# Performance work log

Measured on AMD Instinct MI355X. Metric: run time of the kernel, lower is better.

## Reference

```python
import jax, jax.numpy as jnp
import numpy as np
from jax import lax

B, T, SDIM, ADIM, HDIM, NH, NBLK, MAXT = 4, 512, 64, 32, 512, 8, 6, 4096
DFF = 4 * HDIM
S = 3 * T  # (num_state_tokens + 1) * context_len
DH = HDIM // NH


def _layernorm(x, g, b, eps=1e-5):
    m = jnp.mean(x, axis=-1, keepdims=True)
    v = jnp.mean((x - m) ** 2, axis=-1, keepdims=True)
    return (x - m) * lax.rsqrt(v + eps) * g + b


def setup_inputs() -> dict:
    key = jax.random.key(0)
    ks = iter(jax.random.split(key, 40))

    def nrm(shape, scale=0.02):
        return jax.random.normal(next(ks), shape, jnp.float32) * scale

    inp = {
        "timesteps": jax.random.randint(next(ks), (B, T), 0, MAXT),
        "state_0": jax.random.normal(next(ks), (B, T, SDIM), jnp.float32),
        "state_1": jax.random.normal(next(ks), (B, T, SDIM), jnp.float32),
        "actions": jax.random.normal(next(ks), (B, T, ADIM), jnp.float32),
        # embeddings / input projections
        "time_emb": nrm((MAXT, HDIM)),
        "Ws": nrm((SDIM, HDIM)), "bs": jnp.zeros((HDIM,), jnp.float32),
        "Wa": nrm((ADIM, HDIM)), "ba": jnp.zeros((HDIM,), jnp.float32),
        # stacked per-block transformer params (leading axis = n_blocks)
        "Wq": nrm((NBLK, HDIM, HDIM)), "bq": jnp.zeros((NBLK, HDIM), jnp.float32),
        "Wk": nrm((NBLK, HDIM, HDIM)), "bk": jnp.zeros((NBLK, HDIM), jnp.float32),
        "Wv": nrm((NBLK, HDIM, HDIM)), "bv": jnp.zeros((NBLK, HDIM), jnp.float32),
        "Wo": nrm((NBLK, HDIM, HDIM)), "bo": jnp.zeros((NBLK, HDIM), jnp.float32),
        "W1": nrm((NBLK, HDIM, DFF)), "b1": jnp.zeros((NBLK, DFF), jnp.float32),
        "W2": nrm((NBLK, DFF, HDIM)), "b2": jnp.zeros((NBLK, HDIM), jnp.float32),
        "ln1_g": jnp.ones((NBLK, HDIM), jnp.float32), "ln1_b": jnp.zeros((NBLK, HDIM), jnp.float32),
        "ln2_g": jnp.ones((NBLK, HDIM), jnp.float32), "ln2_b": jnp.zeros((NBLK, HDIM), jnp.float32),
        # embed layernorm + action head
        "eln_g": jnp.ones((HDIM,), jnp.float32), "eln_b": jnp.zeros((HDIM,), jnp.float32),
        "Wp": nrm((HDIM, ADIM)), "bp": jnp.zeros((ADIM,), jnp.float32),
    }
    return inp


def reference(timesteps, state_0, state_1, actions, time_emb, Ws, bs, Wa, ba,
              Wq, bq, Wk, bk, Wv, bv, Wo, bo, W1, b1, W2, b2,
              ln1_g, ln1_b, ln2_g, ln2_b, eln_g, eln_b, Wp, bp):
    te = time_emb[timesteps]                       # (B, T, H)
    s0 = state_0 @ Ws + bs + te                    # shared state embedding
    s1 = state_1 @ Ws + bs + te
    ae = actions @ Wa + ba + te
    # interleave: (B, T, 3, H) -> (B, 3T, H), token order [s0, s1, a] per timestep
    h = jnp.stack([s0, s1, ae], axis=2).reshape(B, S, HDIM)
    h = _layernorm(h, eln_g, eln_b)

    causal = jnp.tril(jnp.ones((S, S), dtype=bool))
    scale = 1.0 / float(DH) ** 0.5

    def block(x, p):
        wq, bq_, wk, bk_, wv, bv_, wo, bo_, w1, b1_, w2, b2_, g1, be1, g2, be2 = p
        q = (x @ wq + bq_).reshape(B, S, NH, DH)
        k = (x @ wk + bk_).reshape(B, S, NH, DH)
        v = (x @ wv + bv_).reshape(B, S, NH, DH)
        scores = jnp.einsum('bihd,bjhd->bhij', q, k) * scale
        scores = jnp.where(causal, scores, -jnp.inf)
        attn = jax.nn.softmax(scores, axis=-1)
        ctx = jnp.einsum('bhij,bjhd->bihd', attn, v).reshape(B, S, HDIM)
        x = x + (ctx @ wo + bo_)
        x = _layernorm(x, g1, be1)
        mlp = jax.nn.gelu(x @ w1 + b1_, approximate=False) @ w2 + b2_
        x = _layernorm(x + mlp, g2, be2)
        return x, None

    h, _ = lax.scan(block, h,
                    (Wq, bq, Wk, bk, Wv, bv, Wo, bo, W1, b1, W2, b2,
                     ln1_g, ln1_b, ln2_g, ln2_b))

    h = h.reshape(B, T, 3, HDIM)                   # (B, T, num_tokens, H)
    act_in = h[:, :, 1]                            # token index -2 = last state token
    return act_in @ Wp + bp                        # (B, T, act_dim)
```

## Files before the change

### kernel.cpp

```cpp
#include <hip/hip_runtime.h>
#include <hip/hip_bf16.h>
#include <math.h>

#define BB 4
#define TT 512
#define SDIM 64
#define ADIM 32
#define HDIM 512
#define NH 8
#define NBLK 6
#define DFF 2048
#define SS 1536
#define DH 64
#define MS (BB*SS)

typedef __attribute__((ext_vector_type(8))) __bf16 bf16x8;
typedef __attribute__((ext_vector_type(4))) float f32x4;

__device__ __forceinline__ __bf16 f2b(float x) { return (__bf16)x; }

__device__ __forceinline__ void gll16(const void* g, void* l) {
    __builtin_amdgcn_global_load_lds(
        (const __attribute__((address_space(1))) unsigned int*)g,
        (__attribute__((address_space(3))) unsigned int*)l, 16, 0, 0);
}

__global__ __launch_bounds__(512) void embed_ln_kernel(
    const int* __restrict__ timesteps,
    const float* __restrict__ state0, const float* __restrict__ state1,
    const float* __restrict__ actions, const float* __restrict__ time_emb,
    const float* __restrict__ Ws, const float* __restrict__ bs,
    const float* __restrict__ Wa, const float* __restrict__ ba,
    const float* __restrict__ eg, const float* __restrict__ eb,
    __bf16* __restrict__ h_bf)
{
    __shared__ float xs[8][64];
    __shared__ float acc_s[8][512];
    __shared__ int tss[8];
    int c = blockIdx.x, t = blockIdx.y, b = blockIdx.z;
    int i0 = c * 8;
    int tid = threadIdx.x;
    int K = (t == 2) ? ADIM : SDIM;
    int ksh = (t == 2) ? 5 : 6;
    const float* W    = (t == 2) ? Wa : Ws;
    const float* bias = (t == 2) ? ba : bs;
    const float* src  = (t == 0) ? state0  + ((size_t)(b*TT + i0)) * SDIM
                      : (t == 1) ? state1  + ((size_t)(b*TT + i0)) * SDIM
                                 : actions + ((size_t)(b*TT + i0)) * ADIM;

    if (tid < 8) tss[tid] = timesteps[b*TT + i0 + tid];
    for (int idx = tid; idx < 8 * K; idx += 512) {
        int r = idx >> ksh, kk = idx & (K - 1);
        xs[r][kk] = src[r * K + kk];
    }
    __syncthreads();

    float acc[8];
    #pragma unroll
    for (int r = 0; r < 8; ++r)
        acc[r] = bias[tid] + time_emb[(size_t)tss[r] * HDIM + tid];
    for (int kk = 0; kk < K; ++kk) {
        float w = W[(size_t)kk * HDIM + tid];
        #pragma unroll
        for (int r = 0; r < 8; ++r) acc[r] += xs[r][kk] * w;
    }
    #pragma unroll
    for (int r = 0; r < 8; ++r) acc_s[r][tid] = acc[r];
    __syncthreads();

    int w = tid >> 6, lane = tid & 63;
    float4 p0 = *(const float4*)&acc_s[w][lane * 8];
    float4 p1 = *(const float4*)&acc_s[w][lane * 8 + 4];
    float v[8] = {p0.x, p0.y, p0.z, p0.w, p1.x, p1.y, p1.z, p1.w};
    float s = 0.f, sq = 0.f;
    #pragma unroll
    for (int u = 0; u < 8; ++u) { s += v[u]; sq += v[u] * v[u]; }
    #pragma unroll
    for (int off = 1; off < 64; off <<= 1) { s += __shfl_xor(s, off); sq += __shfl_xor(sq, off); }
    float mean = s * (1.f / HDIM);
    float var  = sq * (1.f / HDIM) - mean * mean;
    float inv  = rsqrtf(var + 1e-5f);
    float4 g0 = *(const float4*)(eg + lane * 8), g1 = *(const float4*)(eg + lane * 8 + 4);
    float4 b0 = *(const float4*)(eb + lane * 8), b1 = *(const float4*)(eb + lane * 8 + 4);
    float gg[8] = {g0.x, g0.y, g0.z, g0.w, g1.x, g1.y, g1.z, g1.w};
    float bbv[8] = {b0.x, b0.y, b0.z, b0.w, b1.x, b1.y, b1.z, b1.w};
    __bf16 o8[8];
    #pragma unroll
    for (int u = 0; u < 8; ++u) o8[u] = f2b((v[u] - mean) * inv * gg[u] + bbv[u]);
    int row = b * SS + (i0 + w) * 3 + t;
    *(uint4*)(h_bf + (size_t)row * HDIM + lane * 8) = *(uint4*)o8;
}

__global__ __launch_bounds__(256) void ln_add2_kernel(
    __bf16* __restrict__ h_bf, const __bf16* __restrict__ ya,
    const __bf16* __restrict__ yb,
    const float* __restrict__ g, const float* __restrict__ bvec)
{
    int w = threadIdx.x >> 6, lane = threadIdx.x & 63;
    int row = blockIdx.x * 4 + w;
    size_t base = (size_t)row * HDIM + lane * 8;
    bf16x8 h8 = *(const bf16x8*)(h_bf + base);
    bf16x8 a8 = *(const bf16x8*)(ya + base);
    bf16x8 b8 = *(const bf16x8*)(yb + base);
    float v[8], s = 0.f, sq = 0.f;
    #pragma unroll
    for (int u = 0; u < 8; ++u) {
        v[u] = (float)h8[u] + (float)a8[u] + (float)b8[u];
        s += v[u]; sq += v[u] * v[u];
    }
    #pragma unroll
    for (int off = 1; off < 64; off <<= 1) { s += __shfl_xor(s, off); sq += __shfl_xor(sq, off); }
    float mean = s * (1.f / HDIM);
    float var  = sq * (1.f / HDIM) - mean * mean;
    float inv  = rsqrtf(var + 1e-5f);
    float4 g0 = *(const float4*)(g + lane * 8), g1 = *(const float4*)(g + lane * 8 + 4);
    float4 b0 = *(const float4*)(bvec + lane * 8), b1 = *(const float4*)(bvec + lane * 8 + 4);
    float gg[8] = {g0.x, g0.y, g0.z, g0.w, g1.x, g1.y, g1.z, g1.w};
    float bbv[8] = {b0.x, b0.y, b0.z, b0.w, b1.x, b1.y, b1.z, b1.w};
    __bf16 o8[8];
    #pragma unroll
    for (int u = 0; u < 8; ++u) o8[u] = f2b((v[u] - mean) * inv * gg[u] + bbv[u]);
    *(uint4*)(h_bf + base) = *(uint4*)o8;
}

__global__ __launch_bounds__(256) void pack_kernel(
    const float* __restrict__ Wq, const float* __restrict__ Wk,
    const float* __restrict__ Wv, const float* __restrict__ Wo,
    const float* __restrict__ W1, const float* __restrict__ W2,
    const float* __restrict__ bq_, const float* __restrict__ bk_, const float* __restrict__ bv_,
    __bf16* __restrict__ wqkvT, __bf16* __restrict__ woT,
    __bf16* __restrict__ w1T, __bf16* __restrict__ w2T, float* __restrict__ biasq)
{
    int lyr = blockIdx.y;
    const float* wq = Wq + (size_t)lyr * HDIM * HDIM;
    const float* wk = Wk + (size_t)lyr * HDIM * HDIM;
    const float* wv = Wv + (size_t)lyr * HDIM * HDIM;
    const float* wo = Wo + (size_t)lyr * HDIM * HDIM;
    const float* w1 = W1 + (size_t)lyr * HDIM * DFF;
    const float* w2 = W2 + (size_t)lyr * DFF * HDIM;
    const float* bqL = bq_ + (size_t)lyr * HDIM;
    const float* bkL = bk_ + (size_t)lyr * HDIM;
    const float* bvL = bv_ + (size_t)lyr * HDIM;
    wqkvT += (size_t)lyr * 1536 * 512;
    woT   += (size_t)lyr * 512 * 512;
    w1T   += (size_t)lyr * 2048 * 512;
    w2T   += (size_t)lyr * 512 * 2048;
    biasq += (size_t)lyr * 1536;

    int bid = blockIdx.x;
    int tid = threadIdx.x;
    if (bid == 768) {
        for (int i = tid; i < 1536; i += 256)
            biasq[i] = (i < 512) ? bqL[i] : ((i < 1024) ? bkL[i-512] : bvL[i-1024]);
        return;
    }
    __shared__ float Ls[64][65];
    const float* src; __bf16* dst; int K, N, kt, nt;
    if (bid < 192) {
        int sec = bid / 64, t = bid % 64;
        src = (sec == 0) ? wq : (sec == 1) ? wk : wv;
        dst = wqkvT + (size_t)sec * 512 * 512;
        K = 512; N = 512; nt = t >> 3; kt = t & 7;
    } else if (bid < 256) {
        int t = bid - 192; src = wo; dst = woT; K = 512; N = 512; nt = t >> 3; kt = t & 7;
    } else if (bid < 512) {
        int t = bid - 256; src = w1; dst = w1T; K = 512; N = 2048; nt = t >> 3; kt = t & 7;
    } else {
        int t = bid - 512; src = w2; dst = w2T; K = 2048; N = 512; nt = t & 7; kt = t >> 3;
    }
    int k0 = kt * 64, n0 = nt * 64;
    int rr = tid >> 4, cc = (tid & 15) * 4;
    #pragma unroll
    for (int p = 0; p < 4; ++p) {
        float4 v = *(const float4*)(src + (size_t)(k0 + rr + p*16) * N + n0 + cc);
        Ls[rr + p*16][cc] = v.x; Ls[rr + p*16][cc+1] = v.y;
        Ls[rr + p*16][cc+2] = v.z; Ls[rr + p*16][cc+3] = v.w;
    }
    __syncthreads();
    int nn = tid >> 3, kc = (tid & 7) * 8;
    #pragma unroll
    for (int p = 0; p < 2; ++p) {
        __bf16 t8[8];
        #pragma unroll
        for (int t2 = 0; t2 < 8; ++t2) t8[t2] = f2b(Ls[kc + t2][nn + p*32]);
        *(uint4*)(dst + (size_t)(n0 + nn + p*32) * K + k0 + kc) = *(uint4*)t8;
    }
}

template<int MT, bool VTMODE>
__global__ __launch_bounds__(256) void gemm_mfma(
    const __bf16* __restrict__ A, const __bf16* __restrict__ Bt,
    const float* __restrict__ bias, __bf16* __restrict__ C,
    __bf16* __restrict__ VTout,
    int N, int Ksub, int lda, int ldb, int ldc, int gelu, size_t cSplitStride)
{
    constexpr int MI = MT / 32;
    constexpr int SMB = 2*MT*64 + 2*128*64;
    __shared__ __align__(16) char sm[SMB];
    __bf16* As = (__bf16*)sm;
    __bf16* Bs = (__bf16*)(sm + 2*MT*64);
    int tid = threadIdx.x;
    int wave = tid >> 6, lane = tid & 63;
    int l15 = lane & 15, quad = lane >> 4;
    int wy = wave >> 1, wx = wave & 1;
    int m0 = blockIdx.y * MT, n0 = blockIdx.x * 128;
    int zs = blockIdx.z;
    int kbase = zs * Ksub;
    C += (size_t)zs * cSplitStride;

    int srow = lane >> 2;
    int clog = (lane & 3) ^ ((lane >> 3) & 3);
    int pchunk = (quad ^ ((l15 >> 1) & 3)) * 8;

    f32x4 acc[MI][4];
    #pragma unroll
    for (int i = 0; i < MI; ++i)
        #pragma unroll
        for (int j = 0; j < 4; ++j) acc[i][j] = (f32x4){0.f,0.f,0.f,0.f};

    const __bf16* Abase = A  + (size_t)m0 * lda + kbase + clog * 8;
    const __bf16* Bbase = Bt + (size_t)n0 * ldb + kbase + clog * 8;
    int NK = Ksub >> 5;

    #pragma unroll
    for (int q = 0; q < MT/64; ++q) {
        int r0 = (wave * (MT/64) + q) * 16;
        gll16(Abase + (size_t)(r0 + srow) * lda, As + r0*32);
    }
    #pragma unroll
    for (int q = 0; q < 2; ++q) {
        int r0 = (wave * 2 + q) * 16;
        gll16(Bbase + (size_t)(r0 + srow) * ldb, Bs + r0*32);
    }

    for (int kt = 0; kt < NK; ++kt) {
        int buf = kt & 1;
        __syncthreads();
        if (kt + 1 < NK) {
            int k0 = (kt + 1) << 5;
            #pragma unroll
            for (int q = 0; q < MT/64; ++q) {
                int r0 = (wave * (MT/64) + q) * 16;
                gll16(Abase + (size_t)(r0 + srow) * lda + k0, As + ((buf^1)*MT + r0)*32);
            }
            #pragma unroll
            for (int q = 0; q < 2; ++q) {
                int r0 = (wave * 2 + q) * 16;
                gll16(Bbase + (size_t)(r0 + srow) * ldb + k0, Bs + ((buf^1)*128 + r0)*32);
            }
        }
        bf16x8 af[MI], bf[4];
        #pragma unroll
        for (int i = 0; i < MI; ++i)
            af[i] = *(const bf16x8*)&As[(buf*MT + wy*(MT/2) + i*16 + l15)*32 + pchunk];
        #pragma unroll
        for (int j = 0; j < 4; ++j)
            bf[j] = *(const bf16x8*)&Bs[(buf*128 + wx*64 + j*16 + l15)*32 + pchunk];
        #pragma unroll
        for (int i = 0; i < MI; ++i)
            #pragma unroll
            for (int j = 0; j < 4; ++j)
                acc[i][j] = __builtin_amdgcn_mfma_f32_16x16x32_bf16(af[i], bf[j], acc[i][j], 0, 0, 0);
    }

    if (VTMODE && n0 >= 1024) {
        __syncthreads();
        __bf16* T = (__bf16*)sm;
        #pragma unroll
        for (int j = 0; j < 4; ++j) {
            int dl = wx*64 + j*16 + l15;
            float bv = bias[n0 + dl];
            int x31 = dl & 31;
            #pragma unroll
            for (int i = 0; i < MI; ++i) {
                int sc = wy*16 + i*4 + quad;
                int phys = sc ^ x31;
                __bf16 v4[4];
                #pragma unroll
                for (int r = 0; r < 4; ++r) v4[r] = f2b(acc[i][j][r] + bv);
                *(uint2*)(T + dl*128 + phys*4) = *(uint2*)v4;
            }
        }
        __syncthreads();
        int dl = tid >> 1, sh = (tid & 1) * 64;
        int dglob = n0 - 1024 + dl;
        int bb = m0 / SS, srel = m0 - bb*SS;
        __bf16* vb = VTout + ((size_t)(bb*NH + (dglob >> 6)) * 64 + (dglob & 63)) * SS + srel + sh;
        int x31 = dl & 31;
        #pragma unroll
        for (int u = 0; u < 8; ++u) {
            int c0 = (sh >> 2) + u*2;
            uint2 lo = *(const uint2*)(T + dl*128 + ((c0    ) ^ x31)*4);
            uint2 hi = *(const uint2*)(T + dl*128 + ((c0 + 1) ^ x31)*4);
            uint4 o; o.x = lo.x; o.y = lo.y; o.z = hi.x; o.w = hi.y;
            *(uint4*)(vb + u*8) = o;
        }
        return;
    }

    #pragma unroll
    for (int j = 0; j < 4; ++j) {
        int cc = n0 + wx*64 + j*16 + l15;
        float bv = (zs == 0) ? bias[cc] : 0.f;
        #pragma unroll
        for (int i = 0; i < MI; ++i) {
            #pragma unroll
            for (int r = 0; r < 4; ++r) {
                int rr = m0 + wy*(MT/2) + i*16 + quad*4 + r;
                float v = acc[i][j][r] + bv;
                if (gelu) v = 0.5f * v * (1.f + erff(v * 0.70710678118654752f));
                C[(size_t)rr * ldc + cc] = f2b(v);
            }
        }
    }
}

#define SM_C 0.18033688011112042f

__device__ __forceinline__ unsigned pack2bf(float a, float b)
{
    union { __bf16 h[2]; unsigned u; } t;
    t.h[0] = (__bf16)a; t.h[1] = (__bf16)b;
    return t.u;
}

__device__ __forceinline__ bf16x8 ptrans(const float* p0, const float* p1, int lane)
{
    int l15 = lane & 15, quad = lane >> 4;
    unsigned pk0a = pack2bf(p0[0], p0[1]), pk0b = pack2bf(p0[2], p0[3]);
    unsigned pk1a = pack2bf(p1[0], p1[1]), pk1b = pack2bf(p1[2], p1[3]);
    int sA = l15 + (quad & 1) * 32;
    int sB = sA + 16;
    int hi = quad >> 1;
    unsigned a0A = (unsigned)__shfl((int)pk0a, sA);
    unsigned a1A = (unsigned)__shfl((int)pk1a, sA);
    unsigned b0A = (unsigned)__shfl((int)pk0b, sA);
    unsigned b1A = (unsigned)__shfl((int)pk1b, sA);
    unsigned a0B = (unsigned)__shfl((int)pk0a, sB);
    unsigned a1B = (unsigned)__shfl((int)pk1a, sB);
    unsigned b0B = (unsigned)__shfl((int)pk0b, sB);
    unsigned b1B = (unsigned)__shfl((int)pk1b, sB);
    union { unsigned u[4]; bf16x8 v; } pb;
    pb.u[0] = hi ? a1A : a0A;
    pb.u[1] = hi ? b1A : b0A;
    pb.u[2] = hi ? a1B : a0B;
    pb.u[3] = hi ? b1B : b0B;
    return pb.v;
}

__global__ __launch_bounds__(256, 3) void attn_kernel(
    __bf16* qkc, const __bf16* __restrict__ VT)
{
    __shared__ __align__(16) char smem[32768];

    int x = blockIdx.x;
    int region = x >> 8;
    int j = x & 255;
    int i = j >> 5;
    int hb = j & 31;
    int qt = (region == 0) ? (23 - i) : (region == 1) ? (8 + i) : i;
    int h = hb >> 2, b = hb & 3;

    int tid = threadIdx.x;
    int w = tid >> 6, lane = tid & 63;
    int l15 = lane & 15, quad = lane >> 4;
    int qrow0 = qt * 64 + w * 16;

    const __bf16* qp = qkc + (size_t)(b*SS + qrow0 + l15) * 1024 + h*64 + quad*8;
    bf16x8 qf0 = *(const bf16x8*)qp;
    bf16x8 qf1 = *(const bf16x8*)(qp + 32);

    const __bf16* kgbase = qkc + (size_t)(b*SS) * 1024 + 512 + h*64;
    const __bf16* vgbase = VT + (size_t)(b*NH + h) * 64 * SS;
    int srow8 = lane >> 3;
    int clog  = (lane & 7) ^ ((lane >> 3) & 7);
    int sw0 = ((0*4 + quad) ^ (l15 & 7)) * 8;
    int sw1 = ((1*4 + quad) ^ (l15 & 7)) * 8;

    f32x4 o0 = {0.f,0.f,0.f,0.f}, o1 = o0, o2 = o0, o3 = o0;
    float sm_m = -1e30f, sm_l = 0.f;

    int nkt = qt + 1;

    #pragma unroll
    for (int q = 0; q < 2; ++q) {
        int r0 = (w*2 + q) * 8;
        gll16(kgbase + (size_t)(r0 + srow8) * 1024 + clog*8, (__bf16*)smem + r0*64);
        gll16(vgbase + (size_t)(r0 + srow8) * SS   + clog*8, (__bf16*)(smem + 16384) + r0*64);
    }
    __syncthreads();

    for (int jt = 0; jt < nkt; ++jt) {
        int buf = jt & 1;
        const __bf16* Kb = (const __bf16*)(smem + buf * 8192);
        const __bf16* Vb = (const __bf16*)(smem + 16384 + buf * 8192);
        if (jt + 1 < nkt) {
            int kb2 = (jt + 1) * 64;
            __bf16* Kn = (__bf16*)(smem + (buf ^ 1) * 8192);
            __bf16* Vn = (__bf16*)(smem + 16384 + (buf ^ 1) * 8192);
            #pragma unroll
            for (int q = 0; q < 2; ++q) {
                int r0 = (w*2 + q) * 8;
                gll16(kgbase + (size_t)(kb2 + r0 + srow8) * 1024 + clog*8, Kn + r0*64);
                gll16(vgbase + (size_t)(r0 + srow8) * SS + kb2 + clog*8,   Vn + r0*64);
            }
        }
        int kb = jt * 64;

        f32x4 s[4];
        #pragma unroll
        for (int f = 0; f < 4; ++f) {
            bf16x8 k0 = *(const bf16x8*)(Kb + (16*f + l15)*64 + sw0);
            bf16x8 k1 = *(const bf16x8*)(Kb + (16*f + l15)*64 + sw1);
            f32x4 sf = {0.f,0.f,0.f,0.f};
            sf = __builtin_amdgcn_mfma_f32_16x16x32_bf16(k0, qf0, sf, 0, 0, 0);
            sf = __builtin_amdgcn_mfma_f32_16x16x32_bf16(k1, qf1, sf, 0, 0, 0);
            s[f] = sf;
        }

        if (kb + 63 > qrow0) {
            int qrow = qrow0 + l15;
            #pragma unroll
            for (int f = 0; f < 4; ++f)
                #pragma unroll
                for (int r = 0; r < 4; ++r)
                    if (kb + 16*f + quad*4 + r > qrow) s[f][r] = -1e30f;
        }

        float tm = -1e30f;
        #pragma unroll
        for (int f = 0; f < 4; ++f)
            #pragma unroll
            for (int r = 0; r < 4; ++r) tm = fmaxf(tm, s[f][r]);
        tm = fmaxf(tm, __shfl_xor(tm, 16));
        tm = fmaxf(tm, __shfl_xor(tm, 32));
        float mnew = fmaxf(sm_m, tm);
        float alpha = __builtin_amdgcn_exp2f((sm_m - mnew) * SM_C);

        float pp[4][4];
        float rs = 0.f;
        #pragma unroll
        for (int f = 0; f < 4; ++f)
            #pragma unroll
            for (int r = 0; r < 4; ++r) {
                float pv = __builtin_amdgcn_exp2f((s[f][r] - mnew) * SM_C);
                pp[f][r] = pv;
                rs += pv;
            }
        rs += __shfl_xor(rs, 16);
        rs += __shfl_xor(rs, 32);
        sm_l = sm_l * alpha + rs;
        sm_m = mnew;
        o0 *= alpha; o1 *= alpha; o2 *= alpha; o3 *= alpha;

        bf16x8 pb01 = ptrans(pp[0], pp[1], lane);
        bf16x8 pb23 = ptrans(pp[2], pp[3], lane);

        #pragma unroll
        for (int ii = 0; ii < 4; ++ii) {
            bf16x8 va = *(const bf16x8*)(Vb + (16*ii + l15)*64 + sw0);
            bf16x8 vb = *(const bf16x8*)(Vb + (16*ii + l15)*64 + sw1);
            f32x4* op = (ii == 0) ? &o0 : (ii == 1) ? &o1 : (ii == 2) ? &o2 : &o3;
            *op = __builtin_amdgcn_mfma_f32_16x16x32_bf16(va, pb01, *op, 0, 0, 0);
            *op = __builtin_amdgcn_mfma_f32_16x16x32_bf16(vb, pb23, *op, 0, 0, 0);
        }
        __syncthreads();
    }

    float* otw = (float*)smem + w * 16 * 68;
    float inv = 1.f / sm_l;
    #pragma unroll
    for (int r = 0; r < 4; ++r) {
        otw[l15*68 +  0 + quad*4 + r] = o0[r] * inv;
        otw[l15*68 + 16 + quad*4 + r] = o1[r] * inv;
        otw[l15*68 + 32 + quad*4 + r] = o2[r] * inv;
        otw[l15*68 + 48 + quad*4 + r] = o3[r] * inv;
    }
    asm volatile("s_waitcnt lgkmcnt(0)" ::: "memory");
    int row = lane >> 2, ch = (lane & 3) * 16;
    union { __bf16 hh[16]; uint4 q4[2]; } ob;
    #pragma unroll
    for (int t2 = 0; t2 < 16; ++t2) ob.hh[t2] = f2b(otw[row*68 + ch + t2]);
    __bf16* cp = qkc + (size_t)(b*SS + qrow0 + row) * 1024 + h*64 + ch;
    *(uint4*)cp = ob.q4[0];
    *(uint4*)(cp + 8) = ob.q4[1];
}

__global__ __launch_bounds__(256) void proj_kernel(
    const __bf16* __restrict__ h_bf, const float* __restrict__ Wp,
    const float* __restrict__ bp, float* __restrict__ out)
{
    int rid = blockIdx.x * 8 + (threadIdx.x >> 5);
    int col = threadIdx.x & 31;
    int b = rid / TT, i = rid - b * TT;
    const __bf16* x = h_bf + ((size_t)(b*SS) + 3*i + 1) * HDIM;
    float acc = bp[col];
    for (int k8 = 0; k8 < HDIM/8; ++k8) {
        bf16x8 x8 = *(const bf16x8*)(x + k8*8);
        #pragma unroll
        for (int u = 0; u < 8; ++u)
            acc += (float)x8[u] * Wp[(k8*8 + u) * ADIM + col];
    }
    out[(size_t)rid * ADIM + col] = acc;
}

extern "C" void kernel_launch(void* const* d_in, const int* in_sizes, int n_in,
                              void* d_out, int out_size, void* d_ws, size_t ws_size,
                              hipStream_t stream)
{
    (void)in_sizes; (void)n_in; (void)out_size; (void)ws_size;
    const int*   timesteps = (const int*)  d_in[0];
    const float* state0    = (const float*)d_in[1];
    const float* state1    = (const float*)d_in[2];
    const float* actions   = (const float*)d_in[3];
    const float* time_emb  = (const float*)d_in[4];
    const float* Ws  = (const float*)d_in[5];
    const float* bs  = (const float*)d_in[6];
    const float* Wa  = (const float*)d_in[7];
    const float* ba  = (const float*)d_in[8];
    const float* Wq  = (const float*)d_in[9];
    const float* bq  = (const float*)d_in[10];
    const float* Wk  = (const float*)d_in[11];
    const float* bk  = (const float*)d_in[12];
    const float* Wv  = (const float*)d_in[13];
    const float* bv  = (const float*)d_in[14];
    const float* Wo  = (const float*)d_in[15];
    const float* bo  = (const float*)d_in[16];
    const float* W1  = (const float*)d_in[17];
    const float* b1  = (const float*)d_in[18];
    const float* W2  = (const float*)d_in[19];
    const float* b2  = (const float*)d_in[20];
    const float* ln1g = (const float*)d_in[21];
    const float* ln1b = (const float*)d_in[22];
    const float* ln2g = (const float*)d_in[23];
    const float* ln2b = (const float*)d_in[24];
    const float* elng = (const float*)d_in[25];
    const float* elnb = (const float*)d_in[26];
    const float* Wp   = (const float*)d_in[27];
    const float* bp   = (const float*)d_in[28];
    float* out = (float*)d_out;

    const size_t SZ = (size_t)MS * HDIM;
    char* p = (char*)d_ws;
    __bf16* h_bf = (__bf16*)p;           p += SZ * 2;
    __bf16* qk   = (__bf16*)p;           p += (size_t)MS * 1024 * 2;
    __bf16* VT   = (__bf16*)p;           p += SZ * 2;
                      p += SZ * 2;
    __bf16* tmpA = (__bf16*)p;           p += SZ * 2;
    __bf16* tmpB = (__bf16*)p;           p += SZ * 2;
    __bf16* wqkvT = (__bf16*)p;          p += (size_t)NBLK * 1536 * 512 * 2;
    __bf16* woT   = (__bf16*)p;          p += (size_t)NBLK * 512 * 512 * 2;
    __bf16* w1T   = (__bf16*)p;          p += (size_t)NBLK * 2048 * 512 * 2;
    __bf16* w2T   = (__bf16*)p;          p += (size_t)NBLK * 512 * 2048 * 2;
    float*  biasq = (float*)p;           p += (size_t)NBLK * 1536 * 4;
    __bf16* hid   = qk;

    embed_ln_kernel<<<dim3(TT/8, 3, BB), 512, 0, stream>>>(timesteps, state0, state1, actions,
                                                           time_emb, Ws, bs, Wa, ba, elng, elnb, h_bf);

    pack_kernel<<<dim3(769, NBLK), 256, 0, stream>>>(Wq, Wk, Wv, Wo, W1, W2, bq, bk, bv,
                                                     wqkvT, woT, w1T, w2T, biasq);

    dim3 gQKV(1536/128, MS/128, 1);
    dim3 gO  (512/128,  MS/64, 2);
    dim3 gF1 (2048/128, MS/128, 1);

    for (int lyr = 0; lyr < NBLK; ++lyr) {
        const __bf16* wqkvT_l = wqkvT + (size_t)lyr * 1536 * 512;
        const __bf16* woT_l   = woT   + (size_t)lyr * 512 * 512;
        const __bf16* w1T_l   = w1T   + (size_t)lyr * 2048 * 512;
        const __bf16* w2T_l   = w2T   + (size_t)lyr * 512 * 2048;
        const float*  biasq_l = biasq + (size_t)lyr * 1536;

        gemm_mfma<128, true><<<gQKV, 256, 0, stream>>>(h_bf, wqkvT_l, biasq_l, qk, VT,
                                                       1536, 512, 512, 512, 1024, 0, 0);
        attn_kernel<<<dim3(768), 256, 0, stream>>>(qk, VT);
        gemm_mfma<64, false><<<gO, 256, 0, stream>>>(qk, woT_l, bo + lyr*HDIM, tmpA, nullptr,
                                                     512, 256, 1024, 512, 512, 0, SZ);
        ln_add2_kernel<<<MS/4, 256, 0, stream>>>(h_bf, tmpA, tmpB, ln1g + lyr*HDIM, ln1b + lyr*HDIM);
        gemm_mfma<128, false><<<gF1, 256, 0, stream>>>(h_bf, w1T_l, b1 + lyr*DFF, hid, nullptr,
                                                       2048, 512, 512, 512, 2048, 1, 0);
        gemm_mfma<64, false><<<gO, 256, 0, stream>>>(hid, w2T_l, b2 + lyr*HDIM, tmpA, nullptr,
                                                     512, 1024, 2048, 2048, 512, 0, SZ);
        ln_add2_kernel<<<MS/4, 256, 0, stream>>>(h_bf, tmpA, tmpB, ln2g + lyr*HDIM, ln2b + lyr*HDIM);
    }

    proj_kernel<<<(BB*TT)/8, 256, 0, stream>>>(h_bf, Wp, bp, out);
}
```

Measured before the change: 954.4 us.

## Use tanh-GELU approximation, lazy softmax rescale, setprio in attention, drop Wo split-K

Replaces the erf-based GELU with a tanh approximation computed with exp2 and a fast reciprocal. The attention softmax now rescales its running max only when the tile max exceeds the current max by a threshold, and the QK and PV MFMA sections are wrapped in s_setprio. The output projection GEMM no longer splits K across two partial buffers, so the first LayerNorm reads one input instead of two. The tanh GELU departs from the exact erf GELU in the reference and may introduce numerical error.

```diff
diff --git a/kernel.cpp b/kernel.cpp
--- a/kernel.cpp
+++ b/kernel.cpp
@@ -91,7 +91,8 @@
     *(uint4*)(h_bf + (size_t)row * HDIM + lane * 8) = *(uint4*)o8;
 }
 
-__global__ __launch_bounds__(256) void ln_add2_kernel(
+template<bool TWO>
+__global__ __launch_bounds__(256) void ln_add_kernel(
     __bf16* __restrict__ h_bf, const __bf16* __restrict__ ya,
     const __bf16* __restrict__ yb,
     const float* __restrict__ g, const float* __restrict__ bvec)
@@ -101,11 +102,12 @@
     size_t base = (size_t)row * HDIM + lane * 8;
     bf16x8 h8 = *(const bf16x8*)(h_bf + base);
     bf16x8 a8 = *(const bf16x8*)(ya + base);
-    bf16x8 b8 = *(const bf16x8*)(yb + base);
+    bf16x8 b8;
+    if (TWO) b8 = *(const bf16x8*)(yb + base);
     float v[8], s = 0.f, sq = 0.f;
     #pragma unroll
     for (int u = 0; u < 8; ++u) {
-        v[u] = (float)h8[u] + (float)a8[u] + (float)b8[u];
+        v[u] = (float)h8[u] + (float)a8[u] + (TWO ? (float)b8[u] : 0.f);
         s += v[u]; sq += v[u] * v[u];
     }
     #pragma unroll
@@ -308,7 +310,11 @@
             for (int r = 0; r < 4; ++r) {
                 int rr = m0 + wy*(MT/2) + i*16 + quad*4 + r;
                 float v = acc[i][j][r] + bv;
-                if (gelu) v = 0.5f * v * (1.f + erff(v * 0.70710678118654752f));
+                if (gelu) {
+                    float u2 = v * (0.7978845608f + 0.0356774081f * v * v);
+                    float e  = __builtin_amdgcn_exp2f(u2 * 2.885390082f);
+                    v = v * (1.f - __builtin_amdgcn_rcpf(e + 1.f));
+                }
                 C[(size_t)rr * ldc + cc] = f2b(v);
             }
         }
@@ -408,6 +414,7 @@
         int kb = jt * 64;
 
         f32x4 s[4];
+        __builtin_amdgcn_s_setprio(1);
         #pragma unroll
         for (int f = 0; f < 4; ++f) {
             bf16x8 k0 = *(const bf16x8*)(Kb + (16*f + l15)*64 + sw0);
@@ -417,6 +424,7 @@
             sf = __builtin_amdgcn_mfma_f32_16x16x32_bf16(k1, qf1, sf, 0, 0, 0);
             s[f] = sf;
         }
+        __builtin_amdgcn_s_setprio(0);
 
         if (kb + 63 > qrow0) {
             int qrow = qrow0 + l15;
@@ -434,8 +442,14 @@
             for (int r = 0; r < 4; ++r) tm = fmaxf(tm, s[f][r]);
         tm = fmaxf(tm, __shfl_xor(tm, 16));
         tm = fmaxf(tm, __shfl_xor(tm, 32));
-        float mnew = fmaxf(sm_m, tm);
-        float alpha = __builtin_amdgcn_exp2f((sm_m - mnew) * SM_C);
+
+        if (!__all(tm <= sm_m + 64.f)) {
+            float mnew = fmaxf(sm_m, tm);
+            float alpha = __builtin_amdgcn_exp2f((sm_m - mnew) * SM_C);
+            sm_l *= alpha;
+            o0 *= alpha; o1 *= alpha; o2 *= alpha; o3 *= alpha;
+            sm_m = mnew;
+        }
 
         float pp[4][4];
         float rs = 0.f;
@@ -443,19 +457,18 @@
         for (int f = 0; f < 4; ++f)
             #pragma unroll
             for (int r = 0; r < 4; ++r) {
-                float pv = __builtin_amdgcn_exp2f((s[f][r] - mnew) * SM_C);
+                float pv = __builtin_amdgcn_exp2f((s[f][r] - sm_m) * SM_C);
                 pp[f][r] = pv;
                 rs += pv;
             }
         rs += __shfl_xor(rs, 16);
         rs += __shfl_xor(rs, 32);
-        sm_l = sm_l * alpha + rs;
-        sm_m = mnew;
-        o0 *= alpha; o1 *= alpha; o2 *= alpha; o3 *= alpha;
+        sm_l += rs;
 
         bf16x8 pb01 = ptrans(pp[0], pp[1], lane);
         bf16x8 pb23 = ptrans(pp[2], pp[3], lane);
 
+        __builtin_amdgcn_s_setprio(1);
         #pragma unroll
         for (int ii = 0; ii < 4; ++ii) {
             bf16x8 va = *(const bf16x8*)(Vb + (16*ii + l15)*64 + sw0);
@@ -464,6 +477,7 @@
             *op = __builtin_amdgcn_mfma_f32_16x16x32_bf16(va, pb01, *op, 0, 0, 0);
             *op = __builtin_amdgcn_mfma_f32_16x16x32_bf16(vb, pb23, *op, 0, 0, 0);
         }
+        __builtin_amdgcn_s_setprio(0);
         __syncthreads();
     }
 
@@ -562,7 +576,8 @@
                                                      wqkvT, woT, w1T, w2T, biasq);
 
     dim3 gQKV(1536/128, MS/128, 1);
-    dim3 gO  (512/128,  MS/64, 2);
+    dim3 gWO (512/128,  MS/128, 1);
+    dim3 gW2 (512/128,  MS/64, 2);
     dim3 gF1 (2048/128, MS/128, 1);
 
     for (int lyr = 0; lyr < NBLK; ++lyr) {
@@ -575,14 +590,16 @@
         gemm_mfma<128, true><<<gQKV, 256, 0, stream>>>(h_bf, wqkvT_l, biasq_l, qk, VT,
                                                        1536, 512, 512, 512, 1024, 0, 0);
         attn_kernel<<<dim3(768), 256, 0, stream>>>(qk, VT);
-        gemm_mfma<64, false><<<gO, 256, 0, stream>>>(qk, woT_l, bo + lyr*HDIM, tmpA, nullptr,
-                                                     512, 256, 1024, 512, 512, 0, SZ);
-        ln_add2_kernel<<<MS/4, 256, 0, stream>>>(h_bf, tmpA, tmpB, ln1g + lyr*HDIM, ln1b + lyr*HDIM);
+        gemm_mfma<128, false><<<gWO, 256, 0, stream>>>(qk, woT_l, bo + lyr*HDIM, tmpA, nullptr,
+                                                       512, 512, 1024, 512, 512, 0, 0);
+        ln_add_kernel<false><<<MS/4, 256, 0, stream>>>(h_bf, tmpA, nullptr,
+                                                       ln1g + lyr*HDIM, ln1b + lyr*HDIM);
         gemm_mfma<128, false><<<gF1, 256, 0, stream>>>(h_bf, w1T_l, b1 + lyr*DFF, hid, nullptr,
                                                        2048, 512, 512, 512, 2048, 1, 0);
-        gemm_mfma<64, false><<<gO, 256, 0, stream>>>(hid, w2T_l, b2 + lyr*HDIM, tmpA, nullptr,
-                                                     512, 1024, 2048, 2048, 512, 0, SZ);
-        ln_add2_kernel<<<MS/4, 256, 0, stream>>>(h_bf, tmpA, tmpB, ln2g + lyr*HDIM, ln2b + lyr*HDIM);
+        gemm_mfma<64, false><<<gW2, 256, 0, stream>>>(hid, w2T_l, b2 + lyr*HDIM, tmpA, nullptr,
+                                                      512, 1024, 2048, 2048, 512, 0, SZ);
+        ln_add_kernel<true><<<MS/4, 256, 0, stream>>>(h_bf, tmpA, tmpB,
+                                                      ln2g + lyr*HDIM, ln2b + lyr*HDIM);
     }
 
     proj_kernel<<<(BB*TT)/8, 256, 0, stream>>>(h_bf, Wp, bp, out);
```

Result: no change. 953.9 us (-0.1%).
